# Kernel optimization log

Measured on AMD Instinct MI355X. Metric: run time of the kernel, lower is better.

Reference implementation:

```python
import jax, jax.numpy as jnp
import numpy as np

T, B, F = 256, 128, 1600
H1, H2, H3 = 60, 15, 10   # MLP dims
GH = 5                    # GRU hidden size


def setup_inputs() -> dict:
    key = jax.random.key(0)
    ks = jax.random.split(key, 24)
    s = 0.1
    inp = {
        "X":   jax.random.normal(ks[0], (T, B, F), jnp.float32),
        "W1":  jax.random.normal(ks[1], (H1, F), jnp.float32) * s,
        "b1":  jax.random.normal(ks[2], (H1,), jnp.float32) * s,
        "W2":  jax.random.normal(ks[3], (H2, H1), jnp.float32) * s,
        "b2":  jax.random.normal(ks[4], (H2,), jnp.float32) * s,
        "W3":  jax.random.normal(ks[5], (H3, H2), jnp.float32) * s,
        "b3":  jax.random.normal(ks[6], (H3,), jnp.float32) * s,
    }
    in_sizes = [H3, GH, GH]
    k = 7
    for l in range(3):
        inp[f"w_ih{l}"] = jax.random.normal(ks[k], (3 * GH, in_sizes[l]), jnp.float32) * s; k += 1
        inp[f"w_hh{l}"] = jax.random.normal(ks[k], (3 * GH, GH), jnp.float32) * s; k += 1
        inp[f"b_ih{l}"] = jax.random.normal(ks[k], (3 * GH,), jnp.float32) * s; k += 1
        inp[f"b_hh{l}"] = jax.random.normal(ks[k], (3 * GH,), jnp.float32) * s; k += 1
    inp["Wout"] = jax.random.normal(ks[k], (1, GH), jnp.float32) * s; k += 1
    inp["bout"] = jax.random.normal(ks[k], (1,), jnp.float32) * s
    return inp


def _gru_layer(x, w_ih, w_hh, b_ih, b_hh):
    # x: (Bb, Tt, I). Precompute input-side gates for all timesteps.
    gi = jnp.einsum('bti,gi->btg', x, w_ih) + b_ih  # (Bb, Tt, 3H)

    def step(h_prev, gi_t):
        gh = h_prev @ w_hh.T + b_hh                 # (Bb, 3H)
        ir, iz, in_ = jnp.split(gi_t, 3, axis=-1)
        hr, hz, hn = jnp.split(gh, 3, axis=-1)
        r = jax.nn.sigmoid(ir + hr)
        z = jax.nn.sigmoid(iz + hz)
        n = jnp.tanh(in_ + r * hn)
        h = (1.0 - z) * n + z * h_prev
        return h, h

    h0 = jnp.zeros((x.shape[0], w_hh.shape[1]), x.dtype)
    _, ys = jax.lax.scan(step, h0, jnp.swapaxes(gi, 0, 1))  # (Tt, Bb, H)
    return jnp.swapaxes(ys, 0, 1)                            # (Bb, Tt, H)


def reference(X, W1, b1, W2, b2, W3, b3,
              w_ih0, w_hh0, b_ih0, b_hh0,
              w_ih1, w_hh1, b_ih1, b_hh1,
              w_ih2, w_hh2, b_ih2, b_hh2,
              Wout, bout):
    x = jnp.transpose(X, (1, 0, 2))        # (B, T, 1600): GRU batch_first layout
    h = jnp.tanh(x @ W1.T + b1)
    h = jnp.tanh(h @ W2.T + b2)
    h = h @ W3.T + b3                      # (B, T, 10) -- no activation after last MLP layer
    seq = h
    for p in ((w_ih0, w_hh0, b_ih0, b_hh0),
              (w_ih1, w_hh1, b_ih1, b_hh1),
              (w_ih2, w_hh2, b_ih2, b_hh2)):
        seq = _gru_layer(seq, *p)          # (B, T, 5)
    y = jnp.swapaxes(seq, 0, 1)            # (T, B, 5)
    y = y @ Wout.T + bout                  # (T, B, 1)
    return jnp.swapaxes(y, -1, -2)         # (T, 1, B)
```

## Files before the change

### kernel.cpp

```cpp
#include <hip/hip_runtime.h>
#include <hip/hip_bf16.h>


#define T_DIM 256
#define B_DIM 128
#define F_DIM 1600
#define H1_DIM 60
#define H2_DIM 15
#define H3_DIM 10
#define GH 5
#define NSTEP 50
#define CT 32
#define NCH (T_DIM / CT)

#define DPP_SHR5  0x115
#define DPP_SHR10 0x11A

typedef __attribute__((ext_vector_type(8))) short bf16x8;
typedef __attribute__((ext_vector_type(4))) float f32x4;

__device__ __forceinline__ float fast_tanh(float x) {
    float e = __expf(2.0f * x);
    return 1.0f - __fdividef(2.0f, e + 1.0f);
}
__device__ __forceinline__ float fast_sigmoid(float x) {
    return __fdividef(1.0f, 1.0f + __expf(-x));
}
__device__ __forceinline__ ushort f2bf_rn(float x) {
    uint u = __float_as_uint(x);
    u += 0x7fffu + ((u >> 16) & 1u);
    return (ushort)(u >> 16);
}
template <int CTRL>
__device__ __forceinline__ float dppf(float v) {
    return __int_as_float(
        __builtin_amdgcn_mov_dpp(__float_as_int(v), CTRL, 0xf, 0xf, true));
}
__device__ __forceinline__ float bperm(int addr, float v) {
    return __int_as_float(__builtin_amdgcn_ds_bpermute(addr, __float_as_int(v)));
}

__global__ __launch_bounds__(256) void pack_w1_kernel(
    const float* __restrict__ W1, ushort* __restrict__ Wp)
{
    const int s  = blockIdx.x;
    const int t  = threadIdx.x;
    const int nf = t >> 6;
    const int l  = t & 63;
    const int n  = nf * 16 + (l & 15);
    const int g  = l >> 4;

    ushort hi[8], lo[8];
#pragma unroll
    for (int j = 0; j < 8; ++j) {
        const int k = s * 32 + g * 8 + j;
        const float v = (n < H1_DIM) ? W1[n * F_DIM + k] : 0.0f;
        const ushort h = f2bf_rn(v);
        const float hf = __uint_as_float(((uint)h) << 16);
        const float r  = v - hf;
        hi[j] = h;
        lo[j] = (ushort)(__float_as_uint(r) >> 16);
    }
    ushort* dst = Wp + ((size_t)(s * 8 + nf * 2)) * 512 + l * 8;
#pragma unroll
    for (int j = 0; j < 8; ++j) dst[j] = hi[j];
#pragma unroll
    for (int j = 0; j < 8; ++j) dst[512 + j] = lo[j];
}

__global__ __launch_bounds__(256) void mlp_kernel(
    const float* __restrict__ X,
    const ushort* __restrict__ Wp,
    const float* __restrict__ b1,
    const float* __restrict__ W2, const float* __restrict__ b2,
    const float* __restrict__ W3, const float* __restrict__ b3,
    const float* __restrict__ wih0, const float* __restrict__ bih0,
    float* __restrict__ gi0)
{
    __shared__ float red[4 * 4096];

    const int tid  = threadIdx.x;
    const int l    = tid & 63;
    const int w    = __builtin_amdgcn_readfirstlane(tid >> 6);
    const int lm   = l & 15;
    const int g    = l >> 4;
    const int row0 = blockIdx.x * 64;

    f32x4 acc[4][4];
#pragma unroll
    for (int mf = 0; mf < 4; ++mf)
#pragma unroll
        for (int nf = 0; nf < 4; ++nf)
            acc[mf][nf] = (f32x4){0.f, 0.f, 0.f, 0.f};

    const int s0 = (w * NSTEP) >> 2;
    const int s1 = ((w + 1) * NSTEP) >> 2;

    for (int s = s0; s < s1; ++s) {
        bf16x8 bh[4], bl[4];
        const ushort* wp_s = Wp + (size_t)s * 4096 + l * 8;
#pragma unroll
        for (int nf = 0; nf < 4; ++nf) {
            bh[nf] = *(const bf16x8*)(wp_s + (nf * 2 + 0) * 512);
            bl[nf] = *(const bf16x8*)(wp_s + (nf * 2 + 1) * 512);
        }
        bf16x8 a_hi[4], a_lo[4];
#pragma unroll
        for (int mf = 0; mf < 4; ++mf) {
            const float* ap = X + (size_t)(row0 + mf * 16 + lm) * F_DIM + s * 32 + g * 8;
            const float4 x0 = *(const float4*)ap;
            const float4 x1 = *(const float4*)(ap + 4);
            const float xs8[8] = {x0.x, x0.y, x0.z, x0.w, x1.x, x1.y, x1.z, x1.w};
            bf16x8 ah, al;
#pragma unroll
            for (int j = 0; j < 8; ++j) {
                const float v = xs8[j];
                const uint  u = __float_as_uint(v);
                const uint uh = (u + 0x7fffu + ((u >> 16) & 1u)) & 0xffff0000u;
                const float hf = __uint_as_float(uh);
                const float r  = v - hf;
                ah[j] = (short)(uh >> 16);
                al[j] = (short)(__float_as_uint(r) >> 16);
            }
            a_hi[mf] = ah; a_lo[mf] = al;
        }
#pragma unroll
        for (int mf = 0; mf < 4; ++mf)
#pragma unroll
            for (int nf = 0; nf < 4; ++nf) {
                f32x4 c = acc[mf][nf];
                c = __builtin_amdgcn_mfma_f32_16x16x32_bf16(a_lo[mf], bh[nf], c, 0, 0, 0);
                c = __builtin_amdgcn_mfma_f32_16x16x32_bf16(a_hi[mf], bl[nf], c, 0, 0, 0);
                c = __builtin_amdgcn_mfma_f32_16x16x32_bf16(a_hi[mf], bh[nf], c, 0, 0, 0);
                acc[mf][nf] = c;
            }
    }

    float* myred = red + w * 4096;
#pragma unroll
    for (int mf = 0; mf < 4; ++mf)
#pragma unroll
        for (int nf = 0; nf < 4; ++nf)
#pragma unroll
            for (int q = 0; q < 4; ++q)
                myred[(mf * 16 + g * 4 + q) * 64 + nf * 16 + lm] = acc[mf][nf][q];
    __syncthreads();

    float rsum[16];
#pragma unroll
    for (int i = 0; i < 16; ++i) {
        const int p = tid + 256 * i;
        rsum[i] = red[p] + red[4096 + p] + red[8192 + p] + red[12288 + p];
    }
    __syncthreads();
    float* redp = red + 8192;
#pragma unroll
    for (int i = 0; i < 16; ++i) {
        const int p = tid + 256 * i;
        redp[(p >> 6) * 65 + (p & 63)] = rsum[i];
    }
    __syncthreads();
    if (w != 0) return;

    float h1v[H1_DIM];
#pragma unroll
    for (int o = 0; o < H1_DIM; ++o)
        h1v[o] = fast_tanh(redp[l * 65 + o] + b1[o]);

    float h2v[H2_DIM];
#pragma unroll
    for (int j = 0; j < H2_DIM; ++j) {
        float sacc = b2[j];
#pragma unroll
        for (int o = 0; o < H1_DIM; ++o) sacc += W2[j * H1_DIM + o] * h1v[o];
        h2v[j] = fast_tanh(sacc);
    }

    float h3v[H3_DIM];
#pragma unroll
    for (int m = 0; m < H3_DIM; ++m) {
        float sacc = b3[m];
#pragma unroll
        for (int j = 0; j < H2_DIM; ++j) sacc += W3[m * H2_DIM + j] * h2v[j];
        h3v[m] = sacc;
    }

    float gv[15];
#pragma unroll
    for (int q = 0; q < 15; ++q) {
        float sacc = bih0[q];
#pragma unroll
        for (int m = 0; m < H3_DIM; ++m) sacc += wih0[q * H3_DIM + m] * h3v[m];
        gv[q] = sacc;
    }

    const int row = row0 + l;
    float4* dst = (float4*)(gi0 + (size_t)row * 16);
    dst[0] = make_float4(gv[0],  gv[1],  gv[2],  gv[3]);
    dst[1] = make_float4(gv[4],  gv[5],  gv[6],  gv[7]);
    dst[2] = make_float4(gv[8],  gv[9],  gv[10], gv[11]);
    dst[3] = make_float4(gv[12], gv[13], gv[14], 0.0f);
}


#define STAGE(C) do {                                                       \
    const int _cb = (C) & 1;                                                \
    float4 _v0, _v1;                                                        \
    {                                                                       \
        const int _t = lane >> 2, _q = lane & 3;                            \
        _v0 = *(const float4*)(gi0 +                                        \
            ((size_t)(((C) * CT + _t) * B_DIM + b)) * 16 + _q * 4);         \
    }                                                                       \
    {                                                                       \
        const int _f = lane + 64, _t = _f >> 2, _q = _f & 3;                \
        _v1 = *(const float4*)(gi0 +                                        \
            ((size_t)(((C) * CT + _t) * B_DIM + b)) * 16 + _q * 4);         \
    }                                                                       \
    *(float4*)&gbuf[_cb][lane >> 2][(lane & 3) * 4] = _v0;                  \
    *(float4*)&gbuf[_cb][(lane + 64) >> 2][((lane + 64) & 3) * 4] = _v1;    \
} while (0)

#define PREF(CB, TL) do { pre = lptr[(CB) * (CT * 16) + (TL) * 16]; } while (0)

#define GSTEP(S, PREFCODE) do {                                             \
         \
    float aA = bA + pre;                                                    \
    _Pragma("unroll") for (int _j = 0; _j < GH; ++_j)                       \
        aA = fmaf(wi[_j], xn[_j], aA);                                      \
    float aB = fmaf(wh[0], hn[0], bB);                                      \
    _Pragma("unroll") for (int _j = 1; _j < GH; ++_j)                       \
        aB = fmaf(wh[_j], hn[_j], aB);                                      \
    PREFCODE                                                                \
    const float sAv = aA + aB;                                              \
    const float sg  = fast_sigmoid(sAv);                                    \
    const float rn  = dppf<DPP_SHR10>(sg);        \
    const float zn  = dppf<DPP_SHR5>(sg);         \
    if (lane == 48 && (unsigned)((S) - 3) < (unsigned)T_DIM)                \
        out[((S) - 3) * B_DIM + b] = sAv;    \
    const float nv = fast_tanh(fmaf(rn, aB, aA));                           \
    const float hu = fmaf(zn, hm - nv, nv);                                 \
    const bool _valid = (unsigned)((S) - row) < (unsigned)T_DIM;            \
    hm = _valid ? hu : hm;                                                  \
                  \
    _Pragma("unroll") for (int _j = 0; _j < GH; ++_j) {                     \
        hn[_j] = bperm(a_self[_j], hm);                                     \
        xn[_j] = bperm(a_prev[_j], hm);                                     \
    }                                                                       \
} while (0)

__global__ __launch_bounds__(128, 1) void gru_kernel(
    const float* __restrict__ gi0,
    const float* __restrict__ whh0, const float* __restrict__ bhh0,
    const float* __restrict__ wih1, const float* __restrict__ whh1,
    const float* __restrict__ bih1, const float* __restrict__ bhh1,
    const float* __restrict__ wih2, const float* __restrict__ whh2,
    const float* __restrict__ bih2, const float* __restrict__ bhh2,
    const float* __restrict__ Wout, const float* __restrict__ bout,
    float* __restrict__ out)
{
    __shared__ float gbuf[2][CT][16];

    const int tid  = threadIdx.x;
    const int w    = __builtin_amdgcn_readfirstlane(tid >> 6);
    const int lane = tid & 63;
    const int b    = blockIdx.x;

    if (w == 1) {
        STAGE(0);
        __syncthreads();
        for (int c = 0; c < NCH; ++c) {
            if (c + 1 < NCH) STAGE(c + 1);
            __syncthreads();
        }
        return;
    }

    const int row = lane >> 4;
    const int g   = lane & 15;

    float wi[GH], wh[GH];
    float bA = 0.f, bB = 0.f;
#pragma unroll
    for (int j = 0; j < GH; ++j) { wi[j] = 0.f; wh[j] = 0.f; }

    if (row == 0) {
        if (g < 15) {
#pragma unroll
            for (int j = 0; j < GH; ++j) wh[j] = whh0[g * GH + j];
            bB = bhh0[g];
        }
    } else if (row < 3) {
        const float* wip = (row == 1) ? wih1 : wih2;
        const float* whp = (row == 1) ? whh1 : whh2;
        const float* bip = (row == 1) ? bih1 : bih2;
        const float* bhp = (row == 1) ? bhh1 : bhh2;
        if (g < 15) {
#pragma unroll
            for (int j = 0; j < GH; ++j) {
                wi[j] = wip[g * GH + j];
                wh[j] = whp[g * GH + j];
            }
            bA = bip[g];
            bB = bhp[g];
        }
    } else if (g == 0) {
#pragma unroll
        for (int j = 0; j < GH; ++j) wi[j] = Wout[j];
        bA = bout[0];
    }

    int a_self[GH], a_prev[GH];
    const int sbase = row * 16;
    const int pbase = ((row + 3) & 3) * 16;
#pragma unroll
    for (int j = 0; j < GH; ++j) {
        a_self[j] = (sbase + 10 + j) << 2;
        a_prev[j] = (pbase + 10 + j) << 2;
    }

    const float* lptr = &gbuf[0][0][(row == 0) ? g : 15];

    float hn[GH] = {0.f, 0.f, 0.f, 0.f, 0.f};
    float xn[GH] = {0.f, 0.f, 0.f, 0.f, 0.f};
    float hm = 0.f, pre = 0.f;

    __syncthreads();
    PREF(0, 0);

    for (int c = 0; c < NCH; ++c) {
        const int cb = c & 1;
#pragma unroll 2
        for (int tl = 0; tl < CT; ++tl) {
            const int s = c * CT + tl;
            GSTEP(s, if (tl + 1 < CT) { PREF(cb, tl + 1); });
        }
        __syncthreads();
        if (c + 1 < NCH) { PREF((c + 1) & 1, 0); }
    }

    for (int s = T_DIM; s < T_DIM + 3; ++s) {
        GSTEP(s, ;);
    }
}

extern "C" void kernel_launch(void* const* d_in, const int* in_sizes, int n_in,
                              void* d_out, int out_size, void* d_ws, size_t ws_size,
                              hipStream_t stream)
{
    (void)in_sizes; (void)n_in; (void)out_size; (void)ws_size;

    const float* X    = (const float*)d_in[0];
    const float* W1   = (const float*)d_in[1];
    const float* b1   = (const float*)d_in[2];
    const float* W2   = (const float*)d_in[3];
    const float* b2   = (const float*)d_in[4];
    const float* W3   = (const float*)d_in[5];
    const float* b3   = (const float*)d_in[6];
    const float* wih0 = (const float*)d_in[7];
    const float* whh0 = (const float*)d_in[8];
    const float* bih0 = (const float*)d_in[9];
    const float* bhh0 = (const float*)d_in[10];
    const float* wih1 = (const float*)d_in[11];
    const float* whh1 = (const float*)d_in[12];
    const float* bih1 = (const float*)d_in[13];
    const float* bhh1 = (const float*)d_in[14];
    const float* wih2 = (const float*)d_in[15];
    const float* whh2 = (const float*)d_in[16];
    const float* bih2 = (const float*)d_in[17];
    const float* bhh2 = (const float*)d_in[18];
    const float* Wout = (const float*)d_in[19];
    const float* bout = (const float*)d_in[20];

    ushort* Wp  = (ushort*)d_ws;
    float*  gi0 = (float*)((char*)d_ws + 524288);

    pack_w1_kernel<<<NSTEP, 256, 0, stream>>>(W1, Wp);
    mlp_kernel<<<512, 256, 0, stream>>>(X, Wp, b1, W2, b2, W3, b3, wih0, bih0, gi0);
    gru_kernel<<<128, 128, 0, stream>>>(gi0, whh0, bhh0,
                                        wih1, whh1, bih1, bhh1,
                                        wih2, whh2, bih2, bhh2,
                                        Wout, bout, (float*)d_out);
}
```

Before: 115.9 us.

## Pack eight batch rows per GRU block sharing one staging wavefront

```diff
diff --git a/kernel.cpp b/kernel.cpp
--- a/kernel.cpp
+++ b/kernel.cpp
@@ -12,6 +12,7 @@
 #define NSTEP 50
 #define CT 32
 #define NCH (T_DIM / CT)
+#define WB 8
 
 #define DPP_SHR5  0x115
 #define DPP_SHR10 0x11A
@@ -205,22 +206,23 @@
 
 #define STAGE(C) do {                                                       \
     const int _cb = (C) & 1;                                                \
-    float4 _v0, _v1;                                                        \
-    {                                                                       \
-        const int _t = lane >> 2, _q = lane & 3;                            \
-        _v0 = *(const float4*)(gi0 +                                        \
-            ((size_t)(((C) * CT + _t) * B_DIM + b)) * 16 + _q * 4);         \
+    float4 _v[16];                                                          \
+    _Pragma("unroll") for (int _i = 0; _i < 16; ++_i) {                     \
+        const int _f = lane + 64 * _i;                                      \
+        const int _t = _f >> 5, _bb = (_f >> 2) & 7, _q = _f & 3;           \
+        _v[_i] = *(const float4*)(gi0 +                                     \
+            ((size_t)(((C) * CT + _t) * B_DIM + b0 + _bb)) * 16 + _q * 4);  \
     }                                                                       \
-    {                                                                       \
-        const int _f = lane + 64, _t = _f >> 2, _q = _f & 3;                \
-        _v1 = *(const float4*)(gi0 +                                        \
-            ((size_t)(((C) * CT + _t) * B_DIM + b)) * 16 + _q * 4);         \
+    _Pragma("unroll") for (int _i = 0; _i < 16; ++_i) {                     \
+        const int _f = lane + 64 * _i;                                      \
+        const int _t = _f >> 5, _bb = (_f >> 2) & 7, _q = _f & 3;           \
+        *(float4*)&gbuf[_cb][_t][_bb][_q * 4] = _v[_i];                     \
     }                                                                       \
-    *(float4*)&gbuf[_cb][lane >> 2][(lane & 3) * 4] = _v0;                  \
-    *(float4*)&gbuf[_cb][(lane + 64) >> 2][((lane + 64) & 3) * 4] = _v1;    \
 } while (0)
 
-#define PREF(CB, TL) do { pre = lptr[(CB) * (CT * 16) + (TL) * 16]; } while (0)
+#define PREF(CB, TL) do {                                                   \
+    pre = lptr[(CB) * (CT * WB * 16) + (TL) * (WB * 16)];                   \
+} while (0)
 
 #define GSTEP(S, PREFCODE) do {                                             \
          \
@@ -248,7 +250,7 @@
     }                                                                       \
 } while (0)
 
-__global__ __launch_bounds__(128, 1) void gru_kernel(
+__global__ __launch_bounds__(576, 1) void gru_kernel(
     const float* __restrict__ gi0,
     const float* __restrict__ whh0, const float* __restrict__ bhh0,
     const float* __restrict__ wih1, const float* __restrict__ whh1,
@@ -258,14 +260,14 @@
     const float* __restrict__ Wout, const float* __restrict__ bout,
     float* __restrict__ out)
 {
-    __shared__ float gbuf[2][CT][16];
+    __shared__ float gbuf[2][CT][WB][16];
 
     const int tid  = threadIdx.x;
     const int w    = __builtin_amdgcn_readfirstlane(tid >> 6);
     const int lane = tid & 63;
-    const int b    = blockIdx.x;
-
-    if (w == 1) {
+    const int b0   = blockIdx.x * WB;
+
+    if (w == WB) {
         STAGE(0);
         __syncthreads();
         for (int c = 0; c < NCH; ++c) {
@@ -277,6 +279,7 @@
 
     const int row = lane >> 4;
     const int g   = lane & 15;
+    const int b   = b0 + w;
 
     float wi[GH], wh[GH];
     float bA = 0.f, bB = 0.f;
@@ -318,7 +321,7 @@
         a_prev[j] = (pbase + 10 + j) << 2;
     }
 
-    const float* lptr = &gbuf[0][0][(row == 0) ? g : 15];
+    const float* lptr = &gbuf[0][0][w][(row == 0) ? g : 15];
 
     float hn[GH] = {0.f, 0.f, 0.f, 0.f, 0.f};
     float xn[GH] = {0.f, 0.f, 0.f, 0.f, 0.f};
@@ -376,8 +379,8 @@
 
     pack_w1_kernel<<<NSTEP, 256, 0, stream>>>(W1, Wp);
     mlp_kernel<<<512, 256, 0, stream>>>(X, Wp, b1, W2, b2, W3, b3, wih0, bih0, gi0);
-    gru_kernel<<<128, 128, 0, stream>>>(gi0, whh0, bhh0,
-                                        wih1, whh1, bih1, bhh1,
-                                        wih2, whh2, bih2, bhh2,
-                                        Wout, bout, (float*)d_out);
-}
+    gru_kernel<<<16, 576, 0, stream>>>(gi0, whh0, bhh0,
+                                       wih1, whh1, bih1, bhh1,
+                                       wih2, whh2, bih2, bhh2,
+                                       Wout, bout, (float*)d_out);
+}
```

Result: slower. 142.2 us (+22.7%).

## Split MLP GEMM across waves by rows instead of K, prefetch next X slice

Applied to the files above, without the earlier changes.

```diff
diff --git a/kernel.cpp b/kernel.cpp
--- a/kernel.cpp
+++ b/kernel.cpp
@@ -77,7 +77,7 @@
     const float* __restrict__ wih0, const float* __restrict__ bih0,
     float* __restrict__ gi0)
 {
-    __shared__ float red[4 * 4096];
+    __shared__ float redp[64 * 65];
 
     const int tid  = threadIdx.x;
     const int l    = tid & 63;
@@ -86,17 +86,23 @@
     const int g    = l >> 4;
     const int row0 = blockIdx.x * 64;
 
-    f32x4 acc[4][4];
-#pragma unroll
-    for (int mf = 0; mf < 4; ++mf)
-#pragma unroll
-        for (int nf = 0; nf < 4; ++nf)
-            acc[mf][nf] = (f32x4){0.f, 0.f, 0.f, 0.f};
-
-    const int s0 = (w * NSTEP) >> 2;
-    const int s1 = ((w + 1) * NSTEP) >> 2;
-
-    for (int s = s0; s < s1; ++s) {
+    f32x4 acc[4];
+#pragma unroll
+    for (int nf = 0; nf < 4; ++nf)
+        acc[nf] = (f32x4){0.f, 0.f, 0.f, 0.f};
+
+    const float* ap = X + (size_t)(row0 + w * 16 + lm) * F_DIM + g * 8;
+
+    float4 x0 = *(const float4*)(ap);
+    float4 x1 = *(const float4*)(ap + 4);
+
+    for (int s = 0; s < NSTEP; ++s) {
+        float4 n0 = make_float4(0.f, 0.f, 0.f, 0.f);
+        float4 n1 = n0;
+        if (s + 1 < NSTEP) {
+            n0 = *(const float4*)(ap + (s + 1) * 32);
+            n1 = *(const float4*)(ap + (s + 1) * 32 + 4);
+        }
         bf16x8 bh[4], bl[4];
         const ushort* wp_s = Wp + (size_t)s * 4096 + l * 8;
 #pragma unroll
@@ -104,61 +110,34 @@
             bh[nf] = *(const bf16x8*)(wp_s + (nf * 2 + 0) * 512);
             bl[nf] = *(const bf16x8*)(wp_s + (nf * 2 + 1) * 512);
         }
-        bf16x8 a_hi[4], a_lo[4];
-#pragma unroll
-        for (int mf = 0; mf < 4; ++mf) {
-            const float* ap = X + (size_t)(row0 + mf * 16 + lm) * F_DIM + s * 32 + g * 8;
-            const float4 x0 = *(const float4*)ap;
-            const float4 x1 = *(const float4*)(ap + 4);
-            const float xs8[8] = {x0.x, x0.y, x0.z, x0.w, x1.x, x1.y, x1.z, x1.w};
-            bf16x8 ah, al;
-#pragma unroll
-            for (int j = 0; j < 8; ++j) {
-                const float v = xs8[j];
-                const uint  u = __float_as_uint(v);
-                const uint uh = (u + 0x7fffu + ((u >> 16) & 1u)) & 0xffff0000u;
-                const float hf = __uint_as_float(uh);
-                const float r  = v - hf;
-                ah[j] = (short)(uh >> 16);
-                al[j] = (short)(__float_as_uint(r) >> 16);
-            }
-            a_hi[mf] = ah; a_lo[mf] = al;
-        }
-#pragma unroll
-        for (int mf = 0; mf < 4; ++mf)
-#pragma unroll
-            for (int nf = 0; nf < 4; ++nf) {
-                f32x4 c = acc[mf][nf];
-                c = __builtin_amdgcn_mfma_f32_16x16x32_bf16(a_lo[mf], bh[nf], c, 0, 0, 0);
-                c = __builtin_amdgcn_mfma_f32_16x16x32_bf16(a_hi[mf], bl[nf], c, 0, 0, 0);
-                c = __builtin_amdgcn_mfma_f32_16x16x32_bf16(a_hi[mf], bh[nf], c, 0, 0, 0);
-                acc[mf][nf] = c;
-            }
-    }
-
-    float* myred = red + w * 4096;
-#pragma unroll
-    for (int mf = 0; mf < 4; ++mf)
-#pragma unroll
-        for (int nf = 0; nf < 4; ++nf)
-#pragma unroll
-            for (int q = 0; q < 4; ++q)
-                myred[(mf * 16 + g * 4 + q) * 64 + nf * 16 + lm] = acc[mf][nf][q];
-    __syncthreads();
-
-    float rsum[16];
-#pragma unroll
-    for (int i = 0; i < 16; ++i) {
-        const int p = tid + 256 * i;
-        rsum[i] = red[p] + red[4096 + p] + red[8192 + p] + red[12288 + p];
-    }
-    __syncthreads();
-    float* redp = red + 8192;
-#pragma unroll
-    for (int i = 0; i < 16; ++i) {
-        const int p = tid + 256 * i;
-        redp[(p >> 6) * 65 + (p & 63)] = rsum[i];
-    }
+        const float xs8[8] = {x0.x, x0.y, x0.z, x0.w, x1.x, x1.y, x1.z, x1.w};
+        bf16x8 ah, al;
+#pragma unroll
+        for (int j = 0; j < 8; ++j) {
+            const float v = xs8[j];
+            const uint  u = __float_as_uint(v);
+            const uint uh = (u + 0x7fffu + ((u >> 16) & 1u)) & 0xffff0000u;
+            const float hf = __uint_as_float(uh);
+            const float r  = v - hf;
+            ah[j] = (short)(uh >> 16);
+            al[j] = (short)(__float_as_uint(r) >> 16);
+        }
+#pragma unroll
+        for (int nf = 0; nf < 4; ++nf) {
+            f32x4 c = acc[nf];
+            c = __builtin_amdgcn_mfma_f32_16x16x32_bf16(al, bh[nf], c, 0, 0, 0);
+            c = __builtin_amdgcn_mfma_f32_16x16x32_bf16(ah, bl[nf], c, 0, 0, 0);
+            c = __builtin_amdgcn_mfma_f32_16x16x32_bf16(ah, bh[nf], c, 0, 0, 0);
+            acc[nf] = c;
+        }
+        x0 = n0; x1 = n1;
+    }
+
+#pragma unroll
+    for (int nf = 0; nf < 4; ++nf)
+#pragma unroll
+        for (int q = 0; q < 4; ++q)
+            redp[(w * 16 + g * 4 + q) * 65 + nf * 16 + lm] = acc[nf][q];
     __syncthreads();
     if (w != 0) return;
 
```

After: 128.7 us. 11.1% more time.

## Halve MLP block rows and prefetch next X tile in registers

Applied to the files above, without the earlier changes.

```diff
diff --git a/kernel.cpp b/kernel.cpp
--- a/kernel.cpp
+++ b/kernel.cpp
@@ -77,18 +77,18 @@
     const float* __restrict__ wih0, const float* __restrict__ bih0,
     float* __restrict__ gi0)
 {
-    __shared__ float red[4 * 4096];
+    __shared__ float red[4][2048];
 
     const int tid  = threadIdx.x;
     const int l    = tid & 63;
     const int w    = __builtin_amdgcn_readfirstlane(tid >> 6);
     const int lm   = l & 15;
     const int g    = l >> 4;
-    const int row0 = blockIdx.x * 64;
-
-    f32x4 acc[4][4];
-#pragma unroll
-    for (int mf = 0; mf < 4; ++mf)
+    const int row0 = blockIdx.x * 32;
+
+    f32x4 acc[2][4];
+#pragma unroll
+    for (int mf = 0; mf < 2; ++mf)
 #pragma unroll
         for (int nf = 0; nf < 4; ++nf)
             acc[mf][nf] = (f32x4){0.f, 0.f, 0.f, 0.f};
@@ -96,7 +96,30 @@
     const int s0 = (w * NSTEP) >> 2;
     const int s1 = ((w + 1) * NSTEP) >> 2;
 
+    float4 x0[2], x1[2];
+#pragma unroll
+    for (int mf = 0; mf < 2; ++mf) {
+        const float* ap = X + (size_t)(row0 + mf * 16 + lm) * F_DIM + s0 * 32 + g * 8;
+        x0[mf] = *(const float4*)ap;
+        x1[mf] = *(const float4*)(ap + 4);
+    }
+
     for (int s = s0; s < s1; ++s) {
+        float4 n0[2], n1[2];
+#pragma unroll
+        for (int mf = 0; mf < 2; ++mf) {
+            n0[mf] = make_float4(0.f, 0.f, 0.f, 0.f);
+            n1[mf] = n0[mf];
+        }
+        if (s + 1 < s1) {
+#pragma unroll
+            for (int mf = 0; mf < 2; ++mf) {
+                const float* ap = X + (size_t)(row0 + mf * 16 + lm) * F_DIM
+                                + (s + 1) * 32 + g * 8;
+                n0[mf] = *(const float4*)ap;
+                n1[mf] = *(const float4*)(ap + 4);
+            }
+        }
         bf16x8 bh[4], bl[4];
         const ushort* wp_s = Wp + (size_t)s * 4096 + l * 8;
 #pragma unroll
@@ -104,13 +127,10 @@
             bh[nf] = *(const bf16x8*)(wp_s + (nf * 2 + 0) * 512);
             bl[nf] = *(const bf16x8*)(wp_s + (nf * 2 + 1) * 512);
         }
-        bf16x8 a_hi[4], a_lo[4];
-#pragma unroll
-        for (int mf = 0; mf < 4; ++mf) {
-            const float* ap = X + (size_t)(row0 + mf * 16 + lm) * F_DIM + s * 32 + g * 8;
-            const float4 x0 = *(const float4*)ap;
-            const float4 x1 = *(const float4*)(ap + 4);
-            const float xs8[8] = {x0.x, x0.y, x0.z, x0.w, x1.x, x1.y, x1.z, x1.w};
+#pragma unroll
+        for (int mf = 0; mf < 2; ++mf) {
+            const float xs8[8] = {x0[mf].x, x0[mf].y, x0[mf].z, x0[mf].w,
+                                  x1[mf].x, x1[mf].y, x1[mf].z, x1[mf].w};
             bf16x8 ah, al;
 #pragma unroll
             for (int j = 0; j < 8; ++j) {
@@ -122,23 +142,22 @@
                 ah[j] = (short)(uh >> 16);
                 al[j] = (short)(__float_as_uint(r) >> 16);
             }
-            a_hi[mf] = ah; a_lo[mf] = al;
-        }
-#pragma unroll
-        for (int mf = 0; mf < 4; ++mf)
 #pragma unroll
             for (int nf = 0; nf < 4; ++nf) {
                 f32x4 c = acc[mf][nf];
-                c = __builtin_amdgcn_mfma_f32_16x16x32_bf16(a_lo[mf], bh[nf], c, 0, 0, 0);
-                c = __builtin_amdgcn_mfma_f32_16x16x32_bf16(a_hi[mf], bl[nf], c, 0, 0, 0);
-                c = __builtin_amdgcn_mfma_f32_16x16x32_bf16(a_hi[mf], bh[nf], c, 0, 0, 0);
+                c = __builtin_amdgcn_mfma_f32_16x16x32_bf16(al, bh[nf], c, 0, 0, 0);
+                c = __builtin_amdgcn_mfma_f32_16x16x32_bf16(ah, bl[nf], c, 0, 0, 0);
+                c = __builtin_amdgcn_mfma_f32_16x16x32_bf16(ah, bh[nf], c, 0, 0, 0);
                 acc[mf][nf] = c;
             }
-    }
-
-    float* myred = red + w * 4096;
-#pragma unroll
-    for (int mf = 0; mf < 4; ++mf)
+        }
+#pragma unroll
+        for (int mf = 0; mf < 2; ++mf) { x0[mf] = n0[mf]; x1[mf] = n1[mf]; }
+    }
+
+    float* myred = &red[w][0];
+#pragma unroll
+    for (int mf = 0; mf < 2; ++mf)
 #pragma unroll
         for (int nf = 0; nf < 4; ++nf)
 #pragma unroll
@@ -146,21 +165,21 @@
                 myred[(mf * 16 + g * 4 + q) * 64 + nf * 16 + lm] = acc[mf][nf][q];
     __syncthreads();
 
-    float rsum[16];
-#pragma unroll
-    for (int i = 0; i < 16; ++i) {
+    float rsum[8];
+#pragma unroll
+    for (int i = 0; i < 8; ++i) {
         const int p = tid + 256 * i;
-        rsum[i] = red[p] + red[4096 + p] + red[8192 + p] + red[12288 + p];
+        rsum[i] = red[0][p] + red[1][p] + red[2][p] + red[3][p];
     }
     __syncthreads();
-    float* redp = red + 8192;
-#pragma unroll
-    for (int i = 0; i < 16; ++i) {
+    float* redp = &red[2][0];
+#pragma unroll
+    for (int i = 0; i < 8; ++i) {
         const int p = tid + 256 * i;
         redp[(p >> 6) * 65 + (p & 63)] = rsum[i];
     }
     __syncthreads();
-    if (w != 0) return;
+    if (w != 0 || l >= 32) return;
 
     float h1v[H1_DIM];
 #pragma unroll
@@ -375,7 +394,7 @@
     float*  gi0 = (float*)((char*)d_ws + 524288);
 
     pack_w1_kernel<<<NSTEP, 256, 0, stream>>>(W1, Wp);
-    mlp_kernel<<<512, 256, 0, stream>>>(X, Wp, b1, W2, b2, W3, b3, wih0, bih0, gi0);
+    mlp_kernel<<<1024, 256, 0, stream>>>(X, Wp, b1, W2, b2, W3, b3, wih0, bih0, gi0);
     gru_kernel<<<128, 128, 0, stream>>>(gi0, whh0, bhh0,
                                         wih1, whh1, bih1, bhh1,
                                         wih2, whh2, bih2, bhh2,
```

Result: faster. 112.3 us (median of 2 runs) (-3.1%).
